# Performance work log

Measured on AMD Instinct MI355X. Metric: run time of the kernel, lower is better.

The kernel has to match this reference:

```python
import jax, jax.numpy as jnp
import numpy as np

B, S, CIN = 16384, 24, 10
NH, DK, DM = 16, 8, 256
DV = DM // NH  # 16
EPS = 1e-5
T_POS = 1000.0


def _ln(x, g, b):
    mu = jnp.mean(x, axis=-1, keepdims=True)
    var = jnp.mean((x - mu) ** 2, axis=-1, keepdims=True)
    return (x - mu) * jax.lax.rsqrt(var + EPS) * g + b


def _bn(x, g, b, m, v):
    # eval-mode BatchNorm1d over channel (last) dim
    return (x - m) * jax.lax.rsqrt(v + EPS) * g + b


def setup_inputs() -> dict:
    key = jax.random.key(0)
    ks = jax.random.split(key, 16)
    x = jax.random.normal(ks[0], (B, S, CIN + 1), dtype=jnp.float32)
    pos = jax.random.uniform(ks[1], (B, S), dtype=jnp.float32) * 365.0
    x = x.at[:, :, 0].set(pos)
    w = lambda k, shp, s=0.05: (jax.random.normal(k, shp, dtype=jnp.float32) * s)
    d = {
        'x': x,
        'ln1_g': jnp.ones((CIN,), jnp.float32), 'ln1_b': jnp.zeros((CIN,), jnp.float32),
        'conv_w': w(ks[2], (DM, CIN)), 'conv_b': jnp.zeros((DM,), jnp.float32),
        'bn1_g': jnp.ones((DM,), jnp.float32), 'bn1_b': jnp.zeros((DM,), jnp.float32),
        'bn1_m': jnp.zeros((DM,), jnp.float32), 'bn1_v': jnp.ones((DM,), jnp.float32),
        'Q': w(ks[3], (NH, DK), float(np.sqrt(2.0 / DK))),
        'Wk': w(ks[4], (NH * DK, DM), float(np.sqrt(2.0 / DK))), 'bk': jnp.zeros((NH * DK,), jnp.float32),
        'W1': w(ks[5], (128, 256)), 'b1': jnp.zeros((128,), jnp.float32),
        'bn2_g': jnp.ones((128,), jnp.float32), 'bn2_b': jnp.zeros((128,), jnp.float32),
        'bn2_m': jnp.zeros((128,), jnp.float32), 'bn2_v': jnp.ones((128,), jnp.float32),
        'oln_g': jnp.ones((128,), jnp.float32), 'oln_b': jnp.zeros((128,), jnp.float32),
        'Wd1': w(ks[6], (64, 128)), 'bd1': jnp.zeros((64,), jnp.float32),
        'bnd1_g': jnp.ones((64,), jnp.float32), 'bnd1_b': jnp.zeros((64,), jnp.float32),
        'bnd1_m': jnp.zeros((64,), jnp.float32), 'bnd1_v': jnp.ones((64,), jnp.float32),
        'Wd2': w(ks[7], (32, 64)), 'bd2': jnp.zeros((32,), jnp.float32),
        'bnd2_g': jnp.ones((32,), jnp.float32), 'bnd2_b': jnp.zeros((32,), jnp.float32),
        'bnd2_m': jnp.zeros((32,), jnp.float32), 'bnd2_v': jnp.ones((32,), jnp.float32),
        'Wd3': w(ks[8], (20, 32)), 'bd3': jnp.zeros((20,), jnp.float32),
    }
    return d


def reference(x, ln1_g, ln1_b, conv_w, conv_b, bn1_g, bn1_b, bn1_m, bn1_v,
              Q, Wk, bk, W1, b1, bn2_g, bn2_b, bn2_m, bn2_v, oln_g, oln_b,
              Wd1, bd1, bnd1_g, bnd1_b, bnd1_m, bnd1_v,
              Wd2, bd2, bnd2_g, bnd2_b, bnd2_m, bnd2_v, Wd3, bd3):
    pos = x[:, :, 0]            # (B, S) positions
    feat = x[:, :, 1:]          # (B, S, CIN)
    feat = _ln(feat, ln1_g, ln1_b)
    # inconv: 1x1 Conv1d == per-timestep Linear, then eval BatchNorm1d over channels
    h = jnp.einsum('bsc,dc->bsd', feat, conv_w) + conv_b
    h = _bn(h, bn1_g, bn1_b, bn1_m, bn1_v)
    # sinusoid positional encoding, interleaved sin/cos
    div = jnp.exp(jnp.arange(0, DM, 2, dtype=jnp.float32) * (-np.log(T_POS) / DM))  # (DM/2,)
    ang = pos[:, :, None] * div                                   # (B, S, DM/2)
    pe = jnp.stack([jnp.sin(ang), jnp.cos(ang)], axis=-1).reshape(pos.shape[0], pos.shape[1], DM)
    e = h + pe                                                    # (B, S, DM)
    # LTAE multi-head attention with shared learned query
    k = jnp.einsum('bsd,hkd->bshk', e, Wk.reshape(NH, DK, DM)) + bk.reshape(NH, DK)
    logits = jnp.einsum('hk,bshk->bhs', Q, k) / np.sqrt(DK)
    attn = jax.nn.softmax(logits, axis=-1)                        # (B, NH, S); dropout=eval
    v = e.reshape(e.shape[0], e.shape[1], NH, DV)                 # head-chunked values
    o = jnp.einsum('bhs,bshc->bhc', attn, v).reshape(e.shape[0], NH * DV)  # (B, 256)
    # MLP3: Linear(256,128) + BN + ReLU, then dropout(eval) + LayerNorm
    m = jax.nn.relu(_bn(o @ W1.T + b1, bn2_g, bn2_b, bn2_m, bn2_v))
    m = _ln(m, oln_g, oln_b)
    # decoder: [128,64,32,20]
    d1 = jax.nn.relu(_bn(m @ Wd1.T + bd1, bnd1_g, bnd1_b, bnd1_m, bnd1_v))
    d2 = jax.nn.relu(_bn(d1 @ Wd2.T + bd2, bnd2_g, bnd2_b, bnd2_m, bnd2_v))
    out = d2 @ Wd3.T + bd3                                        # (B, 20)
    return out
```

## Files before the change

kernel.cpp:

```cpp
#include <hip/hip_runtime.h>
#include <hip/hip_bf16.h>


typedef __attribute__((ext_vector_type(8))) short bf16x8;
typedef __attribute__((ext_vector_type(4))) float f32x4;

#define EPS 1e-5f
#define INV_SQRT8 0.35355339059327373f
#define KDIV (-0.07785768972392256f)
#define INV2PI 0.15915494309189535f
#define LOG2E 1.4426950408889634f

__device__ __forceinline__ unsigned short f2bf(float f){
  union { float f; unsigned u; } v; v.f = f;
  unsigned r = v.u + 0x7FFFu + ((v.u >> 16) & 1u);
  return (unsigned short)(r >> 16);
}
__device__ __forceinline__ float bf2f(unsigned short h){
  union { unsigned u; float f; } v; v.u = ((unsigned)h) << 16; return v.f;
}
__device__ __forceinline__ float asf(unsigned u){
  union { unsigned u; float f; } v; v.u = u; return v.f;
}
__device__ __forceinline__ unsigned pk2bf(float lo, float hi){
  union { float f; unsigned u; } a, b;
  a.f = lo; b.f = hi;
  return __builtin_amdgcn_perm(b.u + 0x8000u, a.u + 0x8000u, 0x07060302u);
}

__global__ __launch_bounds__(256) void k0_pre(
    const float* __restrict__ conv_w, const float* __restrict__ conv_b,
    const float* __restrict__ bn1_g, const float* __restrict__ bn1_b,
    const float* __restrict__ bn1_m, const float* __restrict__ bn1_v,
    const float* __restrict__ Q, const float* __restrict__ Wk,
    const float* __restrict__ bk,
    const float* __restrict__ W1, const float* __restrict__ b1,
    const float* __restrict__ bn2_g, const float* __restrict__ bn2_b,
    const float* __restrict__ bn2_m, const float* __restrict__ bn2_v,
    const float* __restrict__ oln_g, const float* __restrict__ oln_b,
    const float* __restrict__ Wd1, const float* __restrict__ bd1,
    const float* __restrict__ bnd1_g, const float* __restrict__ bnd1_b,
    const float* __restrict__ bnd1_m, const float* __restrict__ bnd1_v,
    const float* __restrict__ Wd2, const float* __restrict__ bd2,
    const float* __restrict__ bnd2_g, const float* __restrict__ bnd2_b,
    const float* __restrict__ bnd2_m, const float* __restrict__ bnd2_v,
    const float* __restrict__ Wd3,
    unsigned short* __restrict__ wqF, unsigned short* __restrict__ w1F,
    unsigned short* __restrict__ wd1F, unsigned short* __restrict__ wd2F,
    unsigned short* __restrict__ wd3F,
    float* __restrict__ convwT, float* __restrict__ convbE,
    float* __restrict__ biasq, float* __restrict__ b1E,
    float* __restrict__ bd1E, float* __restrict__ bd2E)
{
  __shared__ float redL[256];
  const int t = threadIdx.x;
  const int bid = blockIdx.x;

  if (bid < 64){
    for (int e = bid*512 + t; e < bid*512 + 512; e += 256){
      int j = e & 7, lj = (e >> 3) & 63, kc = (e >> 9) & 7, nt = (e >> 12) & 7;
      int n = nt*16 + (lj & 15);
      int k = kc*32 + ((lj >> 4) << 3) + j;
      float s2 = bn2_g[n] * rsqrtf(bn2_v[n] + EPS);
      w1F[e] = f2bf(W1[n*256 + k] * s2);
    }
  } else if (bid < 68){
    int base = (bid - 64)*2048;
    #pragma unroll 4
    for (int it = 0; it < 8; ++it){
      int e = base + it*256 + t;
      int j = e & 7, lj = (e >> 3) & 63, kc = (e >> 9) & 3, nt = (e >> 11) & 3;
      int n = nt*16 + (lj & 15);
      int k = kc*32 + ((lj >> 4) << 3) + j;
      float sd = bnd1_g[n] * rsqrtf(bnd1_v[n] + EPS);
      wd1F[e] = f2bf(Wd1[n*128 + k] * sd * oln_g[k]);
    }
  } else if (bid == 68){
    #pragma unroll 4
    for (int it = 0; it < 8; ++it){
      int e = it*256 + t;
      int j = e & 7, lj = (e >> 3) & 63, kc = (e >> 9) & 1, nt = (e >> 10) & 1;
      int n = nt*16 + (lj & 15);
      int k = kc*32 + ((lj >> 4) << 3) + j;
      float sd = bnd2_g[n] * rsqrtf(bnd2_v[n] + EPS);
      wd2F[e] = f2bf(Wd2[n*64 + k] * sd);
    }
  } else if (bid == 69){
    #pragma unroll
    for (int it = 0; it < 4; ++it){
      int e = it*256 + t;
      int j = e & 7, lj = (e >> 3) & 63, nt = (e >> 9) & 1;
      int n = nt*16 + (lj & 15);
      int k = ((lj >> 4) << 3) + j;
      float v = (n < 20) ? Wd3[n*32 + k] : 0.f;
      wd3F[e] = f2bf(v);
    }
  } else if (bid == 70 || bid >= 75){
    int c0 = (bid == 70) ? 0 : (bid - 74)*4;
    #pragma unroll
    for (int i2 = 0; i2 < 4; ++i2){
      int e = (c0 + i2)*256 + t;
      int j = e & 7, lj = (e >> 3) & 63, kc = (e >> 9) & 7;
      int h = lj & 15;
      int dd = kc*32 + ((lj >> 4) << 3) + j;
      float acc = 0.f;
      #pragma unroll
      for (int kk = 0; kk < 8; ++kk)
        acc += Q[h*8+kk] * Wk[(h*8+kk)*256 + dd];
      wqF[e] = f2bf(acc * INV_SQRT8);
    }
  } else if (bid == 71){
    __shared__ float wqL[16*257];
    __shared__ float coefL[256*12];
    __shared__ float QL[128];
    __shared__ float bkL[128];
    wqF[4096 + t] = 0; wqF[4096 + 256 + t] = 0;
    if (t < 128){ QL[t] = Q[t]; bkL[t] = bk[t]; }
    __syncthreads();
    {
      const int d = t;
      float s1 = bn1_g[d] * rsqrtf(bn1_v[d] + EPS);
      #pragma unroll
      for (int c = 0; c < 10; ++c) coefL[d*12 + c] = conv_w[d*10 + c] * s1;
      coefL[d*12 + 10] = conv_b[d]*s1 + bn1_b[d] - bn1_m[d]*s1;
      coefL[d*12 + 11] = 0.f;
      #pragma unroll 4
      for (int h = 0; h < 16; ++h){
        float acc = 0.f;
        #pragma unroll
        for (int kk = 0; kk < 8; ++kk)
          acc += QL[h*8+kk] * Wk[(h*8+kk)*256 + d];
        wqL[h*257 + d] = acc;
      }
    }
    __syncthreads();
    if (t < 176){
      int h = t / 11, cc = t - h*11;
      const float* wq = wqL + h*257;
      float acc = 0.f;
      #pragma unroll 4
      for (int d2 = 0; d2 < 256; ++d2)
        acc += coefL[d2*12 + cc] * wq[d2];
      acc *= INV_SQRT8;
      if (cc < 10){
        int lane = (cc < 8) ? h : (16 + h);
        int j = cc & 7;
        wqF[4096 + lane*8 + j] = f2bf(acc);
      } else {
        float qb = 0.f;
        #pragma unroll
        for (int kk = 0; kk < 8; ++kk) qb += QL[h*8+kk]*bkL[h*8+kk];
        biasq[h] = acc + qb * INV_SQRT8;
      }
    }
  } else if (bid == 72){
    #pragma unroll
    for (int it = 0; it < 10; ++it){
      int e = it*256 + t;
      int c = e >> 8, d = e & 255;
      float s1 = bn1_g[d] * rsqrtf(bn1_v[d] + EPS);
      convwT[e] = conv_w[d*10 + c] * s1;
    }
  } else if (bid == 73){
    {
      int d = t;
      float s1 = bn1_g[d] * rsqrtf(bn1_v[d] + EPS);
      convbE[d] = conv_b[d]*s1 + bn1_b[d] - bn1_m[d]*s1;
    }
    if (t < 128){
      float s2 = bn2_g[t] * rsqrtf(bn2_v[t] + EPS);
      b1E[t] = b1[t]*s2 + bn2_b[t] - bn2_m[t]*s2;
    }
    if (t < 32){
      float sd = bnd2_g[t] * rsqrtf(bnd2_v[t] + EPS);
      bd2E[t] = bd2[t]*sd + bnd2_b[t] - bnd2_m[t]*sd;
    }
  } else {
    int n = t >> 2, si = t & 3;
    float acc = 0.f;
    #pragma unroll 8
    for (int i2 = 0; i2 < 32; ++i2){
      int i = si*32 + i2;
      acc += oln_b[i] * Wd1[n*128 + i];
    }
    redL[t] = acc;
    __syncthreads();
    if (t < 64){
      float sd = bnd1_g[t] * rsqrtf(bnd1_v[t] + EPS);
      float a = redL[4*t] + redL[4*t+1] + redL[4*t+2] + redL[4*t+3];
      bd1E[t] = bd1[t]*sd + bnd1_b[t] - bnd1_m[t]*sd + a*sd;
    }
  }
}

__global__ __launch_bounds__(256, 4) void k1_attn(
    const float* __restrict__ x, const float* __restrict__ ln1_g,
    const float* __restrict__ ln1_b,
    const unsigned short* __restrict__ wqF, const float* __restrict__ convwT,
    const float* __restrict__ convbE, const float* __restrict__ biasq,
    unsigned short* __restrict__ o_frag)
{
  __shared__ __align__(16) unsigned short peR[48*264];
  __shared__ __align__(16) float attnF[32*24];
  __shared__ __align__(16) unsigned short featn[48*16];
  __shared__ __align__(16) float divL[128];
  __shared__ __align__(16) float xL[536];
  float* gL = xL;

  const int t = threadIdx.x;
  const int b0 = blockIdx.x * 2;
  const int w = t >> 6, l = t & 63;

  if (t < 132)
    *(float4*)(xL + t*4) = *(const float4*)(x + (size_t)b0*264 + t*4);
  else if (t < 134)
    *(float4*)(xL + 528 + (t-132)*4) = make_float4(0.f,0.f,0.f,0.f);
  if (t < 128) divL[t] = exp2f((float)t * KDIV) * INV2PI;
  __syncthreads();

  {
    const int g = (l >> 4) & 3, rlo = l & 15;
    #pragma unroll
    for (int it = 0; it < 6; ++it){
      int combo = it*4 + w;
      int mt = combo >> 3, kc = combo & 7;
      int row = mt*16 + rlo;
      int run = kc*4 + g;
      float p = xL[row*11];
      unsigned pk[4];
      #pragma unroll
      for (int q = 0; q < 4; ++q){
        float fr = __builtin_amdgcn_fractf(p * divL[run*4 + q]);
        pk[q] = pk2bf(__builtin_amdgcn_sinf(fr), __builtin_amdgcn_cosf(fr));
      }
      *(uint4*)(peR + row*264 + run*8) = make_uint4(pk[0], pk[1], pk[2], pk[3]);
    }
  }
  if (w == 3 && l < 48){
    const float* xr = xL + l*11;
    float f[10]; float mu = 0.f;
    #pragma unroll
    for (int c = 0; c < 10; ++c){ f[c] = xr[1+c]; mu += f[c]; }
    mu *= 0.1f;
    float var = 0.f;
    #pragma unroll
    for (int c = 0; c < 10; ++c){ float dv = f[c]-mu; var += dv*dv; }
    var *= 0.1f;
    float rs = rsqrtf(var + EPS);
    float fn[10];
    #pragma unroll
    for (int c = 0; c < 10; ++c) fn[c] = (f[c]-mu)*rs*ln1_g[c] + ln1_b[c];
    #pragma unroll
    for (int q = 0; q < 5; ++q)
      *(unsigned*)(featn + l*16 + 2*q) = pk2bf(fn[2*q], fn[2*q+1]);
    #pragma unroll
    for (int z = 0; z < 3; ++z)
      *(unsigned*)(featn + l*16 + 10 + 2*z) = 0u;
  }
  __syncthreads();

  const int m = l & 15, g = l >> 4;
  if (w < 3){
    const int mt = w;
    f32x4 acc = {0.f,0.f,0.f,0.f};
    #pragma unroll
    for (int kc = 0; kc < 8; ++kc){
      bf16x8 a = *(const bf16x8*)(peR + (mt*16 + m)*264 + kc*32 + g*8);
      bf16x8 b = *(const bf16x8*)(wqF + ((size_t)(kc*64 + l))*8);
      acc = __builtin_amdgcn_mfma_f32_16x16x32_bf16(a, b, acc, 0, 0, 0);
    }
    {
      const unsigned short* ap = (g < 2) ? (featn + (mt*16 + m)*16 + g*8)
                                         : (const unsigned short*)(xL + 528);
      bf16x8 a = *(const bf16x8*)ap;
      bf16x8 b = *(const bf16x8*)(wqF + ((size_t)(8*64 + l))*8);
      acc = __builtin_amdgcn_mfma_f32_16x16x32_bf16(a, b, acc, 0, 0, 0);
    }
    float bq = biasq[m];
    #pragma unroll
    for (int reg = 0; reg < 4; ++reg){
      int row = mt*16 + g*4 + reg;
      int bb = row >= 24; int s = row - bb*24;
      attnF[(bb*16+m)*24 + s] = acc[reg] + bq;
    }
  }
  __syncthreads();

  {
    const int bh = t >> 3, ln = t & 7;
    float* L = attnF + bh*24;
    float v0 = L[ln], v1 = L[ln+8], v2 = L[ln+16];
    float mx = fmaxf(fmaxf(v0, v1), v2);
    mx = fmaxf(mx, __shfl_xor(mx, 1, 64));
    mx = fmaxf(mx, __shfl_xor(mx, 2, 64));
    mx = fmaxf(mx, __shfl_xor(mx, 4, 64));
    float p0 = exp2f((v0-mx)*LOG2E);
    float p1 = exp2f((v1-mx)*LOG2E);
    float p2 = exp2f((v2-mx)*LOG2E);
    float sm = p0 + p1 + p2;
    sm += __shfl_xor(sm, 1, 64);
    sm += __shfl_xor(sm, 2, 64);
    sm += __shfl_xor(sm, 4, 64);
    float inv = 1.f / sm;
    L[ln] = p0*inv; L[ln+8] = p1*inv; L[ln+16] = p2*inv;
  }
  __syncthreads();

  if (w >= 2){
    const int bb = w - 2;
    const int q = g;
    union { bf16x8 v; unsigned u[4]; } aF;
    if (q < 3){
      const float* ap = attnF + (bb*16 + m)*24 + q*8;
      float4 a0 = *(const float4*)ap;
      float4 a1 = *(const float4*)(ap + 4);
      aF.u[0] = pk2bf(a0.x, a0.y); aF.u[1] = pk2bf(a0.z, a0.w);
      aF.u[2] = pk2bf(a1.x, a1.y); aF.u[3] = pk2bf(a1.z, a1.w);
    } else {
      aF.u[0] = 0u; aF.u[1] = 0u; aF.u[2] = 0u; aF.u[3] = 0u;
    }
    union { bf16x8 v; unsigned short s[8]; } bF;
    #pragma unroll
    for (int j = 0; j < 8; ++j){
      int s = q*8 + j;
      bF.s[j] = (s < 24) ? featn[(bb*24 + s)*16 + m] : (unsigned short)0;
    }
    f32x4 z = {0.f,0.f,0.f,0.f};
    f32x4 ga = __builtin_amdgcn_mfma_f32_16x16x32_bf16(aF.v, bF.v, z, 0,0,0);
    if (m < 12){
      #pragma unroll
      for (int reg = 0; reg < 4; ++reg){
        int h = q*4 + reg;
        gL[(bb*16+h)*12 + m] = ga[reg];
      }
    }
  }

  const int bb7 = t >> 7, dp = t & 127;
  const int d0 = dp*2, h7 = dp >> 3;
  float2 o2; o2.x = 0.f; o2.y = 0.f;
  {
    float A[24];
    const float* Ab = attnF + (bb7*16+h7)*24;
    #pragma unroll
    for (int q4 = 0; q4 < 6; ++q4)
      *(float4*)(A + q4*4) = *(const float4*)(Ab + q4*4);
    const unsigned short* pr = peR + bb7*24*264 + d0;
    #pragma unroll
    for (int s = 0; s < 24; ++s){
      unsigned u = *(const unsigned*)(pr + s*264);
      o2.x += A[s] * asf(u << 16);
      o2.y += A[s] * asf(u & 0xFFFF0000u);
    }
  }
  __syncthreads();

  {
    float2 cb2 = *(const float2*)(convbE + d0);
    o2.x += cb2.x; o2.y += cb2.y;
    const float* gp = gL + (bb7*16+h7)*12;
    #pragma unroll
    for (int c = 0; c < 10; ++c){
      float2 cw = *(const float2*)(convwT + c*256 + d0);
      o2.x += cw.x * gp[c];
      o2.y += cw.y * gp[c];
    }
    const int row = b0 + bb7;
    const int rt = row >> 4, mm = row & 15;
    const int kc = d0 >> 5, gg = (d0 >> 3) & 3, j = d0 & 7;
    *(unsigned*)(o_frag + ((size_t)((rt*8+kc)*64 + gg*16 + mm))*8 + j)
        = pk2bf(o2.x, o2.y);
  }
}

__global__ __launch_bounds__(256, 4) void k2_mlp(
    const unsigned short* __restrict__ o_frag,
    const unsigned short* __restrict__ w1F, const float* __restrict__ b1E,
    const unsigned short* __restrict__ wd1F, const float* __restrict__ bd1E,
    const unsigned short* __restrict__ wd2F, const float* __restrict__ bd2E,
    const unsigned short* __restrict__ wd3F, const float* __restrict__ bd3,
    float* __restrict__ out)
{
  __shared__ float mL[16*132];
  __shared__ unsigned short mh[16*136];
  __shared__ unsigned short d1L[16*72];
  __shared__ unsigned short d2L[16*40];
  __shared__ float redL[64];
  __shared__ float stats[32];

  const int t = threadIdx.x;
  const int w = t >> 6, l = t & 63;
  const size_t rowBase = (size_t)blockIdx.x * 16;
  const int rt = blockIdx.x;
  const int g8  = (l >> 4) << 3;
  const int c15 = l & 15;

  {
    f32x4 acc[2];
    { f32x4 z = {0.f,0.f,0.f,0.f}; acc[0] = z; acc[1] = z; }
    #pragma unroll
    for (int kc = 0; kc < 8; ++kc){
      bf16x8 a = *(const bf16x8*)(o_frag + ((size_t)((rt*8+kc)*64 + l))*8);
      #pragma unroll
      for (int n2 = 0; n2 < 2; ++n2){
        int nt = 2*w + n2;
        bf16x8 b = *(const bf16x8*)(w1F + ((size_t)((nt*8+kc)*64 + l))*8);
        acc[n2] = __builtin_amdgcn_mfma_f32_16x16x32_bf16(a, b, acc[n2], 0,0,0);
      }
    }
    #pragma unroll
    for (int n2 = 0; n2 < 2; ++n2){
      int col = (2*w + n2)*16 + c15;
      float be = b1E[col];
      #pragma unroll
      for (int reg = 0; reg < 4; ++reg){
        int row = ((l>>4)<<2) + reg;
        mL[row*132 + col] = fmaxf(acc[n2][reg] + be, 0.f);
      }
    }
  }
  __syncthreads();

  if (t < 32){
    const float* R = mL + (t>>1)*132 + (t&1)*64;
    float s = 0.f, q = 0.f;
    for (int k = 0; k < 64; ++k){ float v = R[k]; s += v; q += v*v; }
    redL[t*2] = s; redL[t*2+1] = q;
  }
  __syncthreads();
  if (t < 16){
    float s = redL[4*t] + redL[4*t+2];
    float q = redL[4*t+1] + redL[4*t+3];
    float mu = s * (1.f/128.f);
    float var = q * (1.f/128.f) - mu*mu;
    stats[2*t] = mu; stats[2*t+1] = rsqrtf(var + EPS);
  }
  __syncthreads();

  {
    int r = t >> 4, run = t & 15;
    float mu = stats[2*r], rs = stats[2*r+1];
    const float* R = mL + r*132 + run*8;
    unsigned pk[4];
    #pragma unroll
    for (int q = 0; q < 4; ++q)
      pk[q] = pk2bf((R[2*q]-mu)*rs, (R[2*q+1]-mu)*rs);
    *(uint4*)(mh + r*136 + run*8) = make_uint4(pk[0], pk[1], pk[2], pk[3]);
  }
  __syncthreads();

  {
    const int nt = w;
    f32x4 acc = {0.f,0.f,0.f,0.f};
    #pragma unroll
    for (int kc = 0; kc < 4; ++kc){
      bf16x8 b = *(const bf16x8*)(wd1F + ((size_t)((nt*4+kc)*64 + l))*8);
      bf16x8 a = *(const bf16x8*)(mh + c15*136 + kc*32 + g8);
      acc = __builtin_amdgcn_mfma_f32_16x16x32_bf16(a, b, acc, 0,0,0);
    }
    int col = nt*16 + c15;
    float be = bd1E[col];
    #pragma unroll
    for (int reg = 0; reg < 4; ++reg){
      int row = ((l>>4)<<2) + reg;
      d1L[row*72 + col] = f2bf(fmaxf(acc[reg] + be, 0.f));
    }
  }
  __syncthreads();

  if (w < 2){
    const int nt = w;
    f32x4 acc = {0.f,0.f,0.f,0.f};
    #pragma unroll
    for (int kc = 0; kc < 2; ++kc){
      bf16x8 a = *(const bf16x8*)(d1L + c15*72 + kc*32 + g8);
      bf16x8 b = *(const bf16x8*)(wd2F + ((size_t)((nt*2+kc)*64 + l))*8);
      acc = __builtin_amdgcn_mfma_f32_16x16x32_bf16(a, b, acc, 0,0,0);
    }
    int col = nt*16 + c15;
    float be = bd2E[col];
    #pragma unroll
    for (int reg = 0; reg < 4; ++reg){
      int row = ((l>>4)<<2) + reg;
      d2L[row*40 + col] = f2bf(fmaxf(acc[reg] + be, 0.f));
    }
  }
  __syncthreads();

  if (w < 2){
    const int nt = w;
    bf16x8 a = *(const bf16x8*)(d2L + c15*40 + g8);
    bf16x8 b = *(const bf16x8*)(wd3F + ((size_t)(nt*64 + l))*8);
    f32x4 acc = {0.f,0.f,0.f,0.f};
    acc = __builtin_amdgcn_mfma_f32_16x16x32_bf16(a, b, acc, 0,0,0);
    int col = nt*16 + c15;
    if (col < 20){
      float be = bd3[col];
      #pragma unroll
      for (int reg = 0; reg < 4; ++reg){
        int row = ((l>>4)<<2) + reg;
        out[(rowBase + row)*20 + col] = acc[reg] + be;
      }
    }
  }
}

extern "C" void kernel_launch(void* const* d_in, const int* in_sizes, int n_in,
                              void* d_out, int out_size, void* d_ws, size_t ws_size,
                              hipStream_t stream)
{
  (void)in_sizes; (void)n_in; (void)out_size; (void)ws_size;
  const float* x      = (const float*)d_in[0];
  const float* ln1_g  = (const float*)d_in[1];
  const float* ln1_b  = (const float*)d_in[2];
  const float* conv_w = (const float*)d_in[3];
  const float* conv_b = (const float*)d_in[4];
  const float* bn1_g  = (const float*)d_in[5];
  const float* bn1_b  = (const float*)d_in[6];
  const float* bn1_m  = (const float*)d_in[7];
  const float* bn1_v  = (const float*)d_in[8];
  const float* Q      = (const float*)d_in[9];
  const float* Wk     = (const float*)d_in[10];
  const float* bk     = (const float*)d_in[11];
  const float* W1     = (const float*)d_in[12];
  const float* b1     = (const float*)d_in[13];
  const float* bn2_g  = (const float*)d_in[14];
  const float* bn2_b  = (const float*)d_in[15];
  const float* bn2_m  = (const float*)d_in[16];
  const float* bn2_v  = (const float*)d_in[17];
  const float* oln_g  = (const float*)d_in[18];
  const float* oln_b  = (const float*)d_in[19];
  const float* Wd1    = (const float*)d_in[20];
  const float* bd1    = (const float*)d_in[21];
  const float* bnd1_g = (const float*)d_in[22];
  const float* bnd1_b = (const float*)d_in[23];
  const float* bnd1_m = (const float*)d_in[24];
  const float* bnd1_v = (const float*)d_in[25];
  const float* Wd2    = (const float*)d_in[26];
  const float* bd2    = (const float*)d_in[27];
  const float* bnd2_g = (const float*)d_in[28];
  const float* bnd2_b = (const float*)d_in[29];
  const float* bnd2_m = (const float*)d_in[30];
  const float* bnd2_v = (const float*)d_in[31];
  const float* Wd3    = (const float*)d_in[32];
  const float* bd3    = (const float*)d_in[33];

  char* ws = (char*)d_ws;
  unsigned short* wqF  = (unsigned short*)(ws + 0);
  unsigned short* w1F  = (unsigned short*)(ws + 9216);
  unsigned short* wd1F = (unsigned short*)(ws + 74752);
  unsigned short* wd2F = (unsigned short*)(ws + 91136);
  unsigned short* wd3F = (unsigned short*)(ws + 95232);
  float* convwT = (float*)(ws + 97280);
  float* convbE = (float*)(ws + 107520);
  float* biasq  = (float*)(ws + 108544);
  float* b1E    = (float*)(ws + 108608);
  float* bd1E   = (float*)(ws + 109120);
  float* bd2E   = (float*)(ws + 109376);
  unsigned short* o_frag = (unsigned short*)(ws + 109568);

  hipLaunchKernelGGL(k0_pre, dim3(78), dim3(256), 0, stream,
      conv_w, conv_b, bn1_g, bn1_b, bn1_m, bn1_v, Q, Wk, bk,
      W1, b1, bn2_g, bn2_b, bn2_m, bn2_v, oln_g, oln_b,
      Wd1, bd1, bnd1_g, bnd1_b, bnd1_m, bnd1_v,
      Wd2, bd2, bnd2_g, bnd2_b, bnd2_m, bnd2_v, Wd3,
      wqF, w1F, wd1F, wd2F, wd3F, convwT, convbE, biasq, b1E, bd1E, bd2E);

  hipLaunchKernelGGL(k1_attn, dim3(8192), dim3(256), 0, stream,
      x, ln1_g, ln1_b, wqF, convwT, convbE, biasq, o_frag);

  hipLaunchKernelGGL(k2_mlp, dim3(1024), dim3(256), 0, stream,
      o_frag, w1F, b1E, wd1F, bd1E, wd2F, bd2E, wd3F, bd3, (float*)d_out);
}
```

Before: 179.7 us.

## Fuse attention and MLP kernels, keeping per-block attention output in LDS

```diff
diff --git a/kernel.cpp b/kernel.cpp
--- a/kernel.cpp
+++ b/kernel.cpp
@@ -193,205 +193,200 @@
   }
 }
 
-__global__ __launch_bounds__(256, 4) void k1_attn(
+__global__ __launch_bounds__(256, 4) void k1f(
     const float* __restrict__ x, const float* __restrict__ ln1_g,
     const float* __restrict__ ln1_b,
     const unsigned short* __restrict__ wqF, const float* __restrict__ convwT,
     const float* __restrict__ convbE, const float* __restrict__ biasq,
-    unsigned short* __restrict__ o_frag)
-{
-  __shared__ __align__(16) unsigned short peR[48*264];
-  __shared__ __align__(16) float attnF[32*24];
-  __shared__ __align__(16) unsigned short featn[48*16];
-  __shared__ __align__(16) float divL[128];
-  __shared__ __align__(16) float xL[536];
-  float* gL = xL;
-
-  const int t = threadIdx.x;
-  const int b0 = blockIdx.x * 2;
-  const int w = t >> 6, l = t & 63;
-
-  if (t < 132)
-    *(float4*)(xL + t*4) = *(const float4*)(x + (size_t)b0*264 + t*4);
-  else if (t < 134)
-    *(float4*)(xL + 528 + (t-132)*4) = make_float4(0.f,0.f,0.f,0.f);
-  if (t < 128) divL[t] = exp2f((float)t * KDIV) * INV2PI;
-  __syncthreads();
-
-  {
-    const int g = (l >> 4) & 3, rlo = l & 15;
-    #pragma unroll
-    for (int it = 0; it < 6; ++it){
-      int combo = it*4 + w;
-      int mt = combo >> 3, kc = combo & 7;
-      int row = mt*16 + rlo;
-      int run = kc*4 + g;
-      float p = xL[row*11];
-      unsigned pk[4];
-      #pragma unroll
-      for (int q = 0; q < 4; ++q){
-        float fr = __builtin_amdgcn_fractf(p * divL[run*4 + q]);
-        pk[q] = pk2bf(__builtin_amdgcn_sinf(fr), __builtin_amdgcn_cosf(fr));
-      }
-      *(uint4*)(peR + row*264 + run*8) = make_uint4(pk[0], pk[1], pk[2], pk[3]);
-    }
-  }
-  if (w == 3 && l < 48){
-    const float* xr = xL + l*11;
-    float f[10]; float mu = 0.f;
-    #pragma unroll
-    for (int c = 0; c < 10; ++c){ f[c] = xr[1+c]; mu += f[c]; }
-    mu *= 0.1f;
-    float var = 0.f;
-    #pragma unroll
-    for (int c = 0; c < 10; ++c){ float dv = f[c]-mu; var += dv*dv; }
-    var *= 0.1f;
-    float rs = rsqrtf(var + EPS);
-    float fn[10];
-    #pragma unroll
-    for (int c = 0; c < 10; ++c) fn[c] = (f[c]-mu)*rs*ln1_g[c] + ln1_b[c];
-    #pragma unroll
-    for (int q = 0; q < 5; ++q)
-      *(unsigned*)(featn + l*16 + 2*q) = pk2bf(fn[2*q], fn[2*q+1]);
-    #pragma unroll
-    for (int z = 0; z < 3; ++z)
-      *(unsigned*)(featn + l*16 + 10 + 2*z) = 0u;
-  }
-  __syncthreads();
-
-  const int m = l & 15, g = l >> 4;
-  if (w < 3){
-    const int mt = w;
-    f32x4 acc = {0.f,0.f,0.f,0.f};
-    #pragma unroll
-    for (int kc = 0; kc < 8; ++kc){
-      bf16x8 a = *(const bf16x8*)(peR + (mt*16 + m)*264 + kc*32 + g*8);
-      bf16x8 b = *(const bf16x8*)(wqF + ((size_t)(kc*64 + l))*8);
-      acc = __builtin_amdgcn_mfma_f32_16x16x32_bf16(a, b, acc, 0, 0, 0);
-    }
-    {
-      const unsigned short* ap = (g < 2) ? (featn + (mt*16 + m)*16 + g*8)
-                                         : (const unsigned short*)(xL + 528);
-      bf16x8 a = *(const bf16x8*)ap;
-      bf16x8 b = *(const bf16x8*)(wqF + ((size_t)(8*64 + l))*8);
-      acc = __builtin_amdgcn_mfma_f32_16x16x32_bf16(a, b, acc, 0, 0, 0);
-    }
-    float bq = biasq[m];
-    #pragma unroll
-    for (int reg = 0; reg < 4; ++reg){
-      int row = mt*16 + g*4 + reg;
-      int bb = row >= 24; int s = row - bb*24;
-      attnF[(bb*16+m)*24 + s] = acc[reg] + bq;
-    }
-  }
-  __syncthreads();
-
-  {
-    const int bh = t >> 3, ln = t & 7;
-    float* L = attnF + bh*24;
-    float v0 = L[ln], v1 = L[ln+8], v2 = L[ln+16];
-    float mx = fmaxf(fmaxf(v0, v1), v2);
-    mx = fmaxf(mx, __shfl_xor(mx, 1, 64));
-    mx = fmaxf(mx, __shfl_xor(mx, 2, 64));
-    mx = fmaxf(mx, __shfl_xor(mx, 4, 64));
-    float p0 = exp2f((v0-mx)*LOG2E);
-    float p1 = exp2f((v1-mx)*LOG2E);
-    float p2 = exp2f((v2-mx)*LOG2E);
-    float sm = p0 + p1 + p2;
-    sm += __shfl_xor(sm, 1, 64);
-    sm += __shfl_xor(sm, 2, 64);
-    sm += __shfl_xor(sm, 4, 64);
-    float inv = 1.f / sm;
-    L[ln] = p0*inv; L[ln+8] = p1*inv; L[ln+16] = p2*inv;
-  }
-  __syncthreads();
-
-  if (w >= 2){
-    const int bb = w - 2;
-    const int q = g;
-    union { bf16x8 v; unsigned u[4]; } aF;
-    if (q < 3){
-      const float* ap = attnF + (bb*16 + m)*24 + q*8;
-      float4 a0 = *(const float4*)ap;
-      float4 a1 = *(const float4*)(ap + 4);
-      aF.u[0] = pk2bf(a0.x, a0.y); aF.u[1] = pk2bf(a0.z, a0.w);
-      aF.u[2] = pk2bf(a1.x, a1.y); aF.u[3] = pk2bf(a1.z, a1.w);
-    } else {
-      aF.u[0] = 0u; aF.u[1] = 0u; aF.u[2] = 0u; aF.u[3] = 0u;
-    }
-    union { bf16x8 v; unsigned short s[8]; } bF;
-    #pragma unroll
-    for (int j = 0; j < 8; ++j){
-      int s = q*8 + j;
-      bF.s[j] = (s < 24) ? featn[(bb*24 + s)*16 + m] : (unsigned short)0;
-    }
-    f32x4 z = {0.f,0.f,0.f,0.f};
-    f32x4 ga = __builtin_amdgcn_mfma_f32_16x16x32_bf16(aF.v, bF.v, z, 0,0,0);
-    if (m < 12){
-      #pragma unroll
-      for (int reg = 0; reg < 4; ++reg){
-        int h = q*4 + reg;
-        gL[(bb*16+h)*12 + m] = ga[reg];
-      }
-    }
-  }
-
-  const int bb7 = t >> 7, dp = t & 127;
-  const int d0 = dp*2, h7 = dp >> 3;
-  float2 o2; o2.x = 0.f; o2.y = 0.f;
-  {
-    float A[24];
-    const float* Ab = attnF + (bb7*16+h7)*24;
-    #pragma unroll
-    for (int q4 = 0; q4 < 6; ++q4)
-      *(float4*)(A + q4*4) = *(const float4*)(Ab + q4*4);
-    const unsigned short* pr = peR + bb7*24*264 + d0;
-    #pragma unroll
-    for (int s = 0; s < 24; ++s){
-      unsigned u = *(const unsigned*)(pr + s*264);
-      o2.x += A[s] * asf(u << 16);
-      o2.y += A[s] * asf(u & 0xFFFF0000u);
-    }
-  }
-  __syncthreads();
-
-  {
-    float2 cb2 = *(const float2*)(convbE + d0);
-    o2.x += cb2.x; o2.y += cb2.y;
-    const float* gp = gL + (bb7*16+h7)*12;
-    #pragma unroll
-    for (int c = 0; c < 10; ++c){
-      float2 cw = *(const float2*)(convwT + c*256 + d0);
-      o2.x += cw.x * gp[c];
-      o2.y += cw.y * gp[c];
-    }
-    const int row = b0 + bb7;
-    const int rt = row >> 4, mm = row & 15;
-    const int kc = d0 >> 5, gg = (d0 >> 3) & 3, j = d0 & 7;
-    *(unsigned*)(o_frag + ((size_t)((rt*8+kc)*64 + gg*16 + mm))*8 + j)
-        = pk2bf(o2.x, o2.y);
-  }
-}
-
-__global__ __launch_bounds__(256, 4) void k2_mlp(
-    const unsigned short* __restrict__ o_frag,
     const unsigned short* __restrict__ w1F, const float* __restrict__ b1E,
     const unsigned short* __restrict__ wd1F, const float* __restrict__ bd1E,
     const unsigned short* __restrict__ wd2F, const float* __restrict__ bd2E,
     const unsigned short* __restrict__ wd3F, const float* __restrict__ bd3,
     float* __restrict__ out)
 {
-  __shared__ float mL[16*132];
-  __shared__ unsigned short mh[16*136];
-  __shared__ unsigned short d1L[16*72];
-  __shared__ unsigned short d2L[16*40];
-  __shared__ float redL[64];
-  __shared__ float stats[32];
+  __shared__ __align__(16) char smem[40832];
+  unsigned short* peR   = (unsigned short*)(smem);
+  float*          mL    = (float*)(smem);
+  unsigned short* mh    = (unsigned short*)(smem + 8448);
+  unsigned short* d1L   = (unsigned short*)(smem + 12800);
+  unsigned short* d2L   = (unsigned short*)(smem + 15104);
+  float*          redL  = (float*)(smem + 16384);
+  float*          stats = (float*)(smem + 16640);
+  float*          attnF = (float*)(smem + 25344);
+  unsigned short* featn = (unsigned short*)(smem + 28416);
+  float*          divL  = (float*)(smem + 29952);
+  float*          xL    = (float*)(smem + 30464);
+  unsigned short* oL    = (unsigned short*)(smem + 32640);
+  float*          gL    = xL;
 
   const int t = threadIdx.x;
   const int w = t >> 6, l = t & 63;
+  const int m = l & 15, g = l >> 4;
+
+  if (t < 128) divL[t] = exp2f((float)t * KDIV) * INV2PI;
+  if (t < 2) *(float4*)(xL + 528 + t*4) = make_float4(0.f,0.f,0.f,0.f);
+
+  for (int it8 = 0; it8 < 8; ++it8){
+    const size_t b0 = (size_t)blockIdx.x*16 + it8*2;
+    __syncthreads();
+    if (t < 132)
+      *(float4*)(xL + t*4) = *(const float4*)(x + b0*264 + t*4);
+    __syncthreads();
+
+    {
+      const int gg = (l >> 4) & 3, rlo = l & 15;
+      #pragma unroll
+      for (int it = 0; it < 6; ++it){
+        int combo = it*4 + w;
+        int mt = combo >> 3, kc = combo & 7;
+        int row = mt*16 + rlo;
+        int run = kc*4 + gg;
+        float p = xL[row*11];
+        unsigned pk[4];
+        #pragma unroll
+        for (int q = 0; q < 4; ++q){
+          float fr = __builtin_amdgcn_fractf(p * divL[run*4 + q]);
+          pk[q] = pk2bf(__builtin_amdgcn_sinf(fr), __builtin_amdgcn_cosf(fr));
+        }
+        *(uint4*)(peR + row*264 + run*8) = make_uint4(pk[0], pk[1], pk[2], pk[3]);
+      }
+    }
+    if (w == 3 && l < 48){
+      const float* xr = xL + l*11;
+      float f[10]; float mu = 0.f;
+      #pragma unroll
+      for (int c = 0; c < 10; ++c){ f[c] = xr[1+c]; mu += f[c]; }
+      mu *= 0.1f;
+      float var = 0.f;
+      #pragma unroll
+      for (int c = 0; c < 10; ++c){ float dv = f[c]-mu; var += dv*dv; }
+      var *= 0.1f;
+      float rs = rsqrtf(var + EPS);
+      float fn[10];
+      #pragma unroll
+      for (int c = 0; c < 10; ++c) fn[c] = (f[c]-mu)*rs*ln1_g[c] + ln1_b[c];
+      #pragma unroll
+      for (int q = 0; q < 5; ++q)
+        *(unsigned*)(featn + l*16 + 2*q) = pk2bf(fn[2*q], fn[2*q+1]);
+      #pragma unroll
+      for (int z = 0; z < 3; ++z)
+        *(unsigned*)(featn + l*16 + 10 + 2*z) = 0u;
+    }
+    __syncthreads();
+
+    if (w < 3){
+      const int mt = w;
+      f32x4 acc = {0.f,0.f,0.f,0.f};
+      #pragma unroll
+      for (int kc = 0; kc < 8; ++kc){
+        bf16x8 a = *(const bf16x8*)(peR + (mt*16 + m)*264 + kc*32 + g*8);
+        bf16x8 b = *(const bf16x8*)(wqF + ((size_t)(kc*64 + l))*8);
+        acc = __builtin_amdgcn_mfma_f32_16x16x32_bf16(a, b, acc, 0, 0, 0);
+      }
+      {
+        const unsigned short* ap = (g < 2) ? (featn + (mt*16 + m)*16 + g*8)
+                                           : (const unsigned short*)(xL + 528);
+        bf16x8 a = *(const bf16x8*)ap;
+        bf16x8 b = *(const bf16x8*)(wqF + ((size_t)(8*64 + l))*8);
+        acc = __builtin_amdgcn_mfma_f32_16x16x32_bf16(a, b, acc, 0, 0, 0);
+      }
+      float bq = biasq[m];
+      #pragma unroll
+      for (int reg = 0; reg < 4; ++reg){
+        int row = mt*16 + g*4 + reg;
+        int bb = row >= 24; int s = row - bb*24;
+        attnF[(bb*16+m)*24 + s] = acc[reg] + bq;
+      }
+    }
+    __syncthreads();
+
+    {
+      const int bh = t >> 3, ln = t & 7;
+      float* L = attnF + bh*24;
+      float v0 = L[ln], v1 = L[ln+8], v2 = L[ln+16];
+      float mx = fmaxf(fmaxf(v0, v1), v2);
+      mx = fmaxf(mx, __shfl_xor(mx, 1, 64));
+      mx = fmaxf(mx, __shfl_xor(mx, 2, 64));
+      mx = fmaxf(mx, __shfl_xor(mx, 4, 64));
+      float p0 = exp2f((v0-mx)*LOG2E);
+      float p1 = exp2f((v1-mx)*LOG2E);
+      float p2 = exp2f((v2-mx)*LOG2E);
+      float sm = p0 + p1 + p2;
+      sm += __shfl_xor(sm, 1, 64);
+      sm += __shfl_xor(sm, 2, 64);
+      sm += __shfl_xor(sm, 4, 64);
+      float inv = 1.f / sm;
+      L[ln] = p0*inv; L[ln+8] = p1*inv; L[ln+16] = p2*inv;
+    }
+    __syncthreads();
+
+    if (w >= 2){
+      const int bb = w - 2;
+      const int q = g;
+      union { bf16x8 v; unsigned u[4]; } aF;
+      if (q < 3){
+        const float* ap = attnF + (bb*16 + m)*24 + q*8;
+        float4 a0 = *(const float4*)ap;
+        float4 a1 = *(const float4*)(ap + 4);
+        aF.u[0] = pk2bf(a0.x, a0.y); aF.u[1] = pk2bf(a0.z, a0.w);
+        aF.u[2] = pk2bf(a1.x, a1.y); aF.u[3] = pk2bf(a1.z, a1.w);
+      } else {
+        aF.u[0] = 0u; aF.u[1] = 0u; aF.u[2] = 0u; aF.u[3] = 0u;
+      }
+      union { bf16x8 v; unsigned short s[8]; } bF;
+      #pragma unroll
+      for (int j = 0; j < 8; ++j){
+        int s = q*8 + j;
+        bF.s[j] = (s < 24) ? featn[(bb*24 + s)*16 + m] : (unsigned short)0;
+      }
+      f32x4 z = {0.f,0.f,0.f,0.f};
+      f32x4 ga = __builtin_amdgcn_mfma_f32_16x16x32_bf16(aF.v, bF.v, z, 0,0,0);
+      if (m < 12){
+        #pragma unroll
+        for (int reg = 0; reg < 4; ++reg){
+          int h = q*4 + reg;
+          gL[(bb*16+h)*12 + m] = ga[reg];
+        }
+      }
+    }
+
+    const int bb7 = t >> 7, dp = t & 127;
+    const int d0 = dp*2, h7 = dp >> 3;
+    float2 o2; o2.x = 0.f; o2.y = 0.f;
+    {
+      float A[24];
+      const float* Ab = attnF + (bb7*16+h7)*24;
+      #pragma unroll
+      for (int q4 = 0; q4 < 6; ++q4)
+        *(float4*)(A + q4*4) = *(const float4*)(Ab + q4*4);
+      const unsigned short* pr = peR + bb7*24*264 + d0;
+      #pragma unroll
+      for (int s = 0; s < 24; ++s){
+        unsigned u = *(const unsigned*)(pr + s*264);
+        o2.x += A[s] * asf(u << 16);
+        o2.y += A[s] * asf(u & 0xFFFF0000u);
+      }
+    }
+    __syncthreads();
+
+    {
+      float2 cb2 = *(const float2*)(convbE + d0);
+      o2.x += cb2.x; o2.y += cb2.y;
+      const float* gp = gL + (bb7*16+h7)*12;
+      #pragma unroll
+      for (int c = 0; c < 10; ++c){
+        float2 cw = *(const float2*)(convwT + c*256 + d0);
+        o2.x += cw.x * gp[c];
+        o2.y += cw.y * gp[c];
+      }
+      const int mm = it8*2 + bb7;
+      const int kc = d0 >> 5, gg = (d0 >> 3) & 3, j = d0 & 7;
+      *(unsigned*)(oL + ((kc*64 + gg*16 + mm)*8 + j)) = pk2bf(o2.x, o2.y);
+    }
+  }
+  __syncthreads();
+
   const size_t rowBase = (size_t)blockIdx.x * 16;
-  const int rt = blockIdx.x;
   const int g8  = (l >> 4) << 3;
   const int c15 = l & 15;
 
@@ -400,7 +395,7 @@
     { f32x4 z = {0.f,0.f,0.f,0.f}; acc[0] = z; acc[1] = z; }
     #pragma unroll
     for (int kc = 0; kc < 8; ++kc){
-      bf16x8 a = *(const bf16x8*)(o_frag + ((size_t)((rt*8+kc)*64 + l))*8);
+      bf16x8 a = *(const bf16x8*)(oL + (kc*64 + l)*8);
       #pragma unroll
       for (int n2 = 0; n2 < 2; ++n2){
         int nt = 2*w + n2;
@@ -557,7 +552,6 @@
   float* b1E    = (float*)(ws + 108608);
   float* bd1E   = (float*)(ws + 109120);
   float* bd2E   = (float*)(ws + 109376);
-  unsigned short* o_frag = (unsigned short*)(ws + 109568);
 
   hipLaunchKernelGGL(k0_pre, dim3(78), dim3(256), 0, stream,
       conv_w, conv_b, bn1_g, bn1_b, bn1_m, bn1_v, Q, Wk, bk,
@@ -566,9 +560,7 @@
       Wd2, bd2, bnd2_g, bnd2_b, bnd2_m, bnd2_v, Wd3,
       wqF, w1F, wd1F, wd2F, wd3F, convwT, convbE, biasq, b1E, bd1E, bd2E);
 
-  hipLaunchKernelGGL(k1_attn, dim3(8192), dim3(256), 0, stream,
-      x, ln1_g, ln1_b, wqF, convwT, convbE, biasq, o_frag);
-
-  hipLaunchKernelGGL(k2_mlp, dim3(1024), dim3(256), 0, stream,
-      o_frag, w1F, b1E, wd1F, bd1E, wd2F, bd2E, wd3F, bd3, (float*)d_out);
-}
+  hipLaunchKernelGGL(k1f, dim3(1024), dim3(256), 0, stream,
+      x, ln1_g, ln1_b, wqF, convwT, convbE, biasq,
+      w1F, b1E, wd1F, bd1E, wd2F, bd2E, wd3F, bd3, (float*)d_out);
+}
```

Result: no change. 181.4 us (+0.9%).
